# Kernel tuning notes

Measured on AMD Instinct MI355X. Metric: run time of the kernel, lower is better.

The kernel has to match this reference:

```python
import jax, jax.numpy as jnp
import numpy as np

B, N, C_IN, C_OUT, NUM_TYPES = 4, 4096, 128, 64, 5
TEMP = 1.0  # self.temp is undefined in the source; use 1.0


def setup_inputs() -> dict:
    key = jax.random.key(0)
    ks = jax.random.split(key, 9)
    bound_p = np.sqrt(6.0 / (C_IN + C_OUT))
    bound_k = np.sqrt(6.0 / (C_OUT + 1))
    return {
        "node_rep": jax.random.normal(ks[0], (B, N, C_IN), dtype=jnp.float32),
        "adj_matrix": jax.random.uniform(ks[1], (N, N), dtype=jnp.float32),
        "node_type": jax.random.randint(ks[2], (N,), 0, NUM_TYPES),
        "proj_W": jax.random.uniform(ks[3], (C_OUT, C_IN), minval=-bound_p, maxval=bound_p, dtype=jnp.float32),
        "proj_b": jnp.zeros((C_OUT,), dtype=jnp.float32),
        "k_W": jax.random.uniform(ks[4], (NUM_TYPES, C_OUT), minval=-bound_k, maxval=bound_k, dtype=jnp.float32),
        "k_b": jnp.zeros((NUM_TYPES,), dtype=jnp.float32),
        "v_W": jax.random.uniform(ks[5], (NUM_TYPES, C_OUT), minval=-bound_k, maxval=bound_k, dtype=jnp.float32),
        "v_b": jnp.zeros((NUM_TYPES,), dtype=jnp.float32),
    }


def reference(node_rep, adj_matrix, node_type, proj_W, proj_b, k_W, k_b, v_W, v_b):
    # projection: [B,N,c_in] -> [B,N,c_out]
    h = jnp.einsum('bnc,oc->bno', node_rep, proj_W) + proj_b
    # per-type scalar scores stacked: [B,N,num_types]
    ks = jnp.einsum('bno,to->bnt', h, k_W) + k_b
    vs = jnp.einsum('bno,to->bnt', h, v_W) + v_b
    # gather score of each node's own type -> [B,N,1]
    idx = jnp.broadcast_to(node_type[None, :, None], (h.shape[0], h.shape[1], 1))
    f1 = jnp.take_along_axis(ks, idx, axis=2)           # [B,N,1]
    f2 = jnp.take_along_axis(vs, idx, axis=2)           # [B,N,1]
    # pairwise logits masked/weighted by adjacency: [B,N,N]
    attn_logits = adj_matrix[None, :, :] * (f1 + jnp.swapaxes(f2, 1, 2))
    unnorm = jax.nn.sigmoid(attn_logits) - 0.5
    attn_probs = jax.nn.softmax(unnorm / TEMP, axis=1)  # softmax over dim 1, as in source
    # aggregate: [B,N,N] @ [B,N,c_out] -> [B,N,c_out]
    return jnp.matmul(attn_probs, h)
```

## Files before the change

kernel.cpp:

```cpp
#include <hip/hip_runtime.h>
#include <hip/hip_bf16.h>
#include <stdint.h>

#define NN   4096
#define BB   4
#define CIN  128
#define COUT 64
#define JSPL 4

typedef __attribute__((ext_vector_type(4))) float f32x4;
typedef __attribute__((ext_vector_type(8))) short s16x8;
typedef __attribute__((ext_vector_type(4))) int   i32x4;

__device__ __forceinline__ float sig_exp(float u) {
    const float L = 1.4426950408889634f;
    float e0 = __builtin_amdgcn_exp2f(-u * L);
    float sg = __builtin_amdgcn_rcpf(1.0f + e0);
    return __builtin_amdgcn_exp2f(__builtin_fmaf(sg, L, -0.7213475204444817f));
}

__device__ __forceinline__ short f2bf(float x) {
    unsigned u = __builtin_bit_cast(unsigned, x);
    return (short)((u + 0x8000u) >> 16);
}

__global__ __launch_bounds__(256) void k_proj(
    const float* __restrict__ node_rep, const int* __restrict__ node_type,
    const float* __restrict__ pW, const float* __restrict__ pb,
    const float* __restrict__ kW, const float* __restrict__ kb,
    const float* __restrict__ vW, const float* __restrict__ vb,
    float* __restrict__ h, float* __restrict__ f1, float* __restrict__ f2,
    float* __restrict__ denom)
{
    if (blockIdx.x < (BB * NN) / 256)
        denom[blockIdx.x * 256 + threadIdx.x] = 0.0f;

    int row = blockIdx.x * 4 + (threadIdx.x >> 6);
    int o   = threadIdx.x & 63;
    int n   = row & (NN - 1);

    const f32x4* xr = (const f32x4*)(node_rep + (size_t)row * CIN);
    const f32x4* wr = (const f32x4*)(pW + (size_t)o * CIN);
    float a0 = pb[o], a1 = 0.f, a2 = 0.f, a3 = 0.f;
    #pragma unroll
    for (int c = 0; c < CIN / 4; ++c) {
        f32x4 x = xr[c], w = wr[c];
        a0 = fmaf(x[0], w[0], a0);
        a1 = fmaf(x[1], w[1], a1);
        a2 = fmaf(x[2], w[2], a2);
        a3 = fmaf(x[3], w[3], a3);
    }
    float acc = (a0 + a1) + (a2 + a3);
    h[(size_t)row * COUT + o] = acc;

    int t = node_type[n];
    float s1 = acc * kW[t * COUT + o];
    float s2 = acc * vW[t * COUT + o];
    #pragma unroll
    for (int off = 32; off; off >>= 1) {
        s1 += __shfl_xor(s1, off, 64);
        s2 += __shfl_xor(s2, off, 64);
    }
    if (o == 0) { f1[row] = s1 + kb[t]; f2[row] = s2 + vb[t]; }
}

__global__ __launch_bounds__(256) void k_denom(
    const float* __restrict__ adj, const float* __restrict__ f1,
    const float* __restrict__ f2, float* __restrict__ denom)
{
    int j4 = blockIdx.x * 1024 + threadIdx.x * 4;
    int i0 = blockIdx.y * 16;

    f32x4 f2r[BB], acc[BB];
    #pragma unroll
    for (int b = 0; b < BB; ++b) {
        f2r[b] = *(const f32x4*)(f2 + b * NN + j4);
        acc[b] = (f32x4){0.f, 0.f, 0.f, 0.f};
    }

    const float* abase = adj + (size_t)i0 * NN + j4;
    f32x4 aA = *(const f32x4*)(abase);
    for (int ii = 0; ii < 16; ii += 2) {
        f32x4 aB = *(const f32x4*)(abase + (size_t)(ii + 1) * NN);
        #pragma unroll
        for (int b = 0; b < BB; ++b) {
            float fv = f1[b * NN + i0 + ii];
            #pragma unroll
            for (int q = 0; q < 4; ++q) acc[b][q] += sig_exp(aA[q] * (fv + f2r[b][q]));
        }
        if (ii + 2 < 16) aA = *(const f32x4*)(abase + (size_t)(ii + 2) * NN);
        #pragma unroll
        for (int b = 0; b < BB; ++b) {
            float fv = f1[b * NN + i0 + ii + 1];
            #pragma unroll
            for (int q = 0; q < 4; ++q) acc[b][q] += sig_exp(aB[q] * (fv + f2r[b][q]));
        }
    }
    #pragma unroll
    for (int b = 0; b < BB; ++b)
        #pragma unroll
        for (int q = 0; q < 4; ++q)
            atomicAdd(&denom[b * NN + j4 + q], acc[b][q]);
}

__global__ __launch_bounds__(256) void k_hst(
    const float* __restrict__ h, const float* __restrict__ denom,
    unsigned short* __restrict__ hsT)
{
    int b  = blockIdx.y;
    int j0 = blockIdx.x * 64;
    __shared__ float tile[64][65];
    int cx = threadIdx.x & 63;
    int ry = threadIdx.x >> 6;
    #pragma unroll
    for (int k = 0; k < 16; ++k) {
        int jl = k * 4 + ry;
        float rd = __builtin_amdgcn_rcpf(denom[b * NN + j0 + jl]);
        tile[jl][cx] = h[((size_t)b * NN + j0 + jl) * COUT + cx] * rd;
    }
    __syncthreads();
    #pragma unroll
    for (int k = 0; k < 16; ++k) {
        int cl = k * 4 + ry;
        hsT[((size_t)b * COUT + cl) * NN + j0 + cx] = (unsigned short)f2bf(tile[cx][cl]);
    }
}

__global__ __launch_bounds__(256, 4) void k_out(
    const float* __restrict__ adj, const float* __restrict__ f1,
    const float* __restrict__ f2, const unsigned short* __restrict__ hsT,
    float* __restrict__ pout)
{
    int i0   = blockIdx.x * 16;
    int jsp  = blockIdx.y;
    int b    = threadIdx.x >> 6;
    int lane = threadIdx.x & 63;
    int lrow = lane & 15;
    int lgrp = lane >> 4;

    const float*          arow = adj + (size_t)(i0 + lrow) * NN;
    const float*          f2b  = f2 + b * NN;
    const unsigned short* hsb  = hsT + ((size_t)b * COUT + lrow) * NN;
    float f1v = f1[b * NN + i0 + lrow];

    f32x4 acc0 = {0.f, 0.f, 0.f, 0.f};
    f32x4 acc1 = acc0, acc2 = acc0, acc3 = acc0;

    int jb = jsp * (NN / JSPL) + lgrp * 8;

#define LDAH(t, a0, a1, h0, h1, h2, h3) {                                  \
    int jk = jb + (t) * 32;                                                \
    a0 = *(const f32x4*)(arow + jk);                                       \
    a1 = *(const f32x4*)(arow + jk + 4);                                   \
    h0 = *(const i32x4*)(hsb + jk);                                        \
    h1 = *(const i32x4*)(hsb + (size_t)16 * NN + jk);                      \
    h2 = *(const i32x4*)(hsb + (size_t)32 * NN + jk);                      \
    h3 = *(const i32x4*)(hsb + (size_t)48 * NN + jk); }

#define COMP(t, a0, a1, h0, h1, h2, h3) {                                  \
    int jk = jb + (t) * 32;                                                \
    f32x4 s0 = *(const f32x4*)(f2b + jk);                                  \
    f32x4 s1 = *(const f32x4*)(f2b + jk + 4);                              \
    float e0 = sig_exp(a0[0] * (f1v + s0[0]));                             \
    float e1 = sig_exp(a0[1] * (f1v + s0[1]));                             \
    float e2 = sig_exp(a0[2] * (f1v + s0[2]));                             \
    float e3 = sig_exp(a0[3] * (f1v + s0[3]));                             \
    float e4 = sig_exp(a1[0] * (f1v + s1[0]));                             \
    float e5 = sig_exp(a1[1] * (f1v + s1[1]));                             \
    float e6 = sig_exp(a1[2] * (f1v + s1[2]));                             \
    float e7 = sig_exp(a1[3] * (f1v + s1[3]));                             \
    s16x8 af;                                                              \
    af[0] = f2bf(e0); af[1] = f2bf(e1); af[2] = f2bf(e2); af[3] = f2bf(e3);\
    af[4] = f2bf(e4); af[5] = f2bf(e5); af[6] = f2bf(e6); af[7] = f2bf(e7);\
    acc0 = __builtin_amdgcn_mfma_f32_16x16x32_bf16(af, __builtin_bit_cast(s16x8, h0), acc0, 0, 0, 0); \
    acc1 = __builtin_amdgcn_mfma_f32_16x16x32_bf16(af, __builtin_bit_cast(s16x8, h1), acc1, 0, 0, 0); \
    acc2 = __builtin_amdgcn_mfma_f32_16x16x32_bf16(af, __builtin_bit_cast(s16x8, h2), acc2, 0, 0, 0); \
    acc3 = __builtin_amdgcn_mfma_f32_16x16x32_bf16(af, __builtin_bit_cast(s16x8, h3), acc3, 0, 0, 0); }

    f32x4 Aa0, Aa1, Ba0, Ba1;
    i32x4 Ah0, Ah1, Ah2, Ah3, Bh0, Bh1, Bh2, Bh3;
    const int T = NN / JSPL / 32;
    LDAH(0, Aa0, Aa1, Ah0, Ah1, Ah2, Ah3);
    for (int t = 0; t < T; t += 2) {
        LDAH(t + 1, Ba0, Ba1, Bh0, Bh1, Bh2, Bh3);
        COMP(t, Aa0, Aa1, Ah0, Ah1, Ah2, Ah3);
        if (t + 2 < T) LDAH(t + 2, Aa0, Aa1, Ah0, Ah1, Ah2, Ah3);
        COMP(t + 1, Ba0, Ba1, Bh0, Bh1, Bh2, Bh3);
    }
#undef LDAH
#undef COMP

    #pragma unroll
    for (int r = 0; r < 4; ++r) {
        float* orow = pout + ((size_t)(jsp * BB + b) * NN + i0 + lgrp * 4 + r) * COUT + lrow;
        orow[ 0] = acc0[r];
        orow[16] = acc1[r];
        orow[32] = acc2[r];
        orow[48] = acc3[r];
    }
}

__global__ __launch_bounds__(256) void k_ored(
    const float* __restrict__ pout, float* __restrict__ out)
{
    size_t e = ((size_t)blockIdx.x * 256 + threadIdx.x) * 4;
    f32x4 s = *(const f32x4*)(pout + e);
    #pragma unroll
    for (int sp = 1; sp < JSPL; ++sp)
        s += *(const f32x4*)(pout + (size_t)sp * BB * NN * COUT + e);
    *(f32x4*)(out + e) = s;
}

extern "C" void kernel_launch(void* const* d_in, const int* in_sizes, int n_in,
                              void* d_out, int out_size, void* d_ws, size_t ws_size,
                              hipStream_t stream)
{
    const float* node_rep = (const float*)d_in[0];
    const float* adj      = (const float*)d_in[1];
    const int*   ntype    = (const int*)  d_in[2];
    const float* pW       = (const float*)d_in[3];
    const float* pb       = (const float*)d_in[4];
    const float* kW       = (const float*)d_in[5];
    const float* kb       = (const float*)d_in[6];
    const float* vW       = (const float*)d_in[7];
    const float* vb       = (const float*)d_in[8];
    float* out = (float*)d_out;

    char* w = (char*)d_ws;
    float*          h     = (float*)(w);
    float*          f1    = (float*)(w + 4194304);
    float*          f2    = (float*)(w + 4259840);
    float*          denom = (float*)(w + 4325376);
    unsigned short* hsT   = (unsigned short*)(w + 4390912);
    float*          pout  = (float*)(w + 6488064);

    k_proj <<<BB * NN / 4, 256, 0, stream>>>(node_rep, ntype, pW, pb, kW, kb, vW, vb, h, f1, f2, denom);
    k_denom<<<dim3(NN / 1024, NN / 16), 256, 0, stream>>>(adj, f1, f2, denom);
    k_hst  <<<dim3(NN / 64, BB), 256, 0, stream>>>(h, denom, hsT);
    k_out  <<<dim3(NN / 16, JSPL), 256, 0, stream>>>(adj, f1, f2, hsT, pout);
    k_ored <<<BB * NN * COUT / 1024, 256, 0, stream>>>(pout, out);
}
```

Measured before the change: 344.8 us.

## Materialize bf16 attention weights once and consume them with an MFMA GEMM

Adds a path that computes the exp(sigmoid) weights once, writes them to workspace as a bf16 matrix, and accumulates per-block partial column sums. A separate reduction kernel replaces the atomic denominator accumulation. A dedicated bf16 MFMA GEMM then multiplies the stored weights by the normalized, transposed h. This removes the second pass of transcendental work in the output kernel, at the cost of writing and reading about 128MB of extra traffic. The new path runs only if the workspace is large enough; otherwise the old kernels run.

Result: faster. 300.1 us (-13.0%).

```diff
diff --git a/kernel.cpp b/kernel.cpp
--- a/kernel.cpp
+++ b/kernel.cpp
@@ -8,9 +8,10 @@
 #define COUT 64
 #define JSPL 4
 
-typedef __attribute__((ext_vector_type(4))) float f32x4;
-typedef __attribute__((ext_vector_type(8))) short s16x8;
-typedef __attribute__((ext_vector_type(4))) int   i32x4;
+typedef __attribute__((ext_vector_type(4))) float          f32x4;
+typedef __attribute__((ext_vector_type(8))) short          s16x8;
+typedef __attribute__((ext_vector_type(4))) int            i32x4;
+typedef __attribute__((ext_vector_type(4))) unsigned short u16x4;
 
 __device__ __forceinline__ float sig_exp(float u) {
     const float L = 1.4426950408889634f;
@@ -63,6 +64,156 @@
     }
     if (o == 0) { f1[row] = s1 + kb[t]; f2[row] = s2 + vb[t]; }
 }
+
+
+__global__ __launch_bounds__(256) void k_emit(
+    const float* __restrict__ adj, const float* __restrict__ f1,
+    const float* __restrict__ f2, unsigned short* __restrict__ E,
+    float* __restrict__ pd)
+{
+    int j4 = blockIdx.x * 1024 + threadIdx.x * 4;
+    int i0 = blockIdx.y * 16;
+
+    f32x4 f2r[BB], acc[BB];
+    #pragma unroll
+    for (int b = 0; b < BB; ++b) {
+        f2r[b] = *(const f32x4*)(f2 + b * NN + j4);
+        acc[b] = (f32x4){0.f, 0.f, 0.f, 0.f};
+    }
+
+    const float* abase = adj + (size_t)i0 * NN + j4;
+    f32x4 cur = *(const f32x4*)(abase);
+    f32x4 nxt = *(const f32x4*)(abase + NN);
+
+    for (int ii = 0; ii < 16; ++ii) {
+        f32x4 a = cur;
+        cur = nxt;
+        if (ii + 2 < 16) nxt = *(const f32x4*)(abase + (size_t)(ii + 2) * NN);
+        int i = i0 + ii;
+        #pragma unroll
+        for (int b = 0; b < BB; ++b) {
+            float fv = f1[b * NN + i];
+            u16x4 ev;
+            #pragma unroll
+            for (int q = 0; q < 4; ++q) {
+                float e = sig_exp(a[q] * (fv + f2r[b][q]));
+                acc[b][q] += e;
+                ev[q] = (unsigned short)f2bf(e);
+            }
+            *(u16x4*)(E + ((size_t)b * NN + i) * NN + j4) = ev;
+        }
+    }
+    #pragma unroll
+    for (int b = 0; b < BB; ++b)
+        *(f32x4*)(pd + (size_t)(blockIdx.y * BB + b) * NN + j4) = acc[b];
+}
+
+__global__ __launch_bounds__(256) void k_dred(
+    const float* __restrict__ pd, float* __restrict__ rden)
+{
+    int gid = blockIdx.x * 256 + threadIdx.x;
+    float s0 = 0.f, s1 = 0.f, s2 = 0.f, s3 = 0.f;
+    for (int it = 0; it < 256; it += 4) {
+        s0 += pd[(size_t)(it + 0) * BB * NN + gid];
+        s1 += pd[(size_t)(it + 1) * BB * NN + gid];
+        s2 += pd[(size_t)(it + 2) * BB * NN + gid];
+        s3 += pd[(size_t)(it + 3) * BB * NN + gid];
+    }
+    rden[gid] = 1.0f / ((s0 + s1) + (s2 + s3));
+}
+
+__global__ __launch_bounds__(256) void k_hst_mul(
+    const float* __restrict__ h, const float* __restrict__ rden,
+    unsigned short* __restrict__ hsT)
+{
+    int b  = blockIdx.y;
+    int j0 = blockIdx.x * 64;
+    __shared__ float tile[64][65];
+    int cx = threadIdx.x & 63;
+    int ry = threadIdx.x >> 6;
+    #pragma unroll
+    for (int k = 0; k < 16; ++k) {
+        int jl = k * 4 + ry;
+        tile[jl][cx] = h[((size_t)b * NN + j0 + jl) * COUT + cx] * rden[b * NN + j0 + jl];
+    }
+    __syncthreads();
+    #pragma unroll
+    for (int k = 0; k < 16; ++k) {
+        int cl = k * 4 + ry;
+        hsT[((size_t)b * COUT + cl) * NN + j0 + cx] = (unsigned short)f2bf(tile[cx][cl]);
+    }
+}
+
+__global__ __launch_bounds__(512) void k_gemm(
+    const unsigned short* __restrict__ E, const unsigned short* __restrict__ hsT,
+    float* __restrict__ out)
+{
+    int i0   = blockIdx.x * 16;
+    int b    = blockIdx.y;
+    int tid  = threadIdx.x;
+    int wid  = tid >> 6;
+    int lane = tid & 63;
+    int lrow = lane & 15;
+    int lgrp = lane >> 4;
+
+    const unsigned short* ea  = E   + ((size_t)b * NN + i0 + lrow) * NN;
+    const unsigned short* hsb = hsT + ((size_t)b * COUT + lrow) * NN;
+
+    f32x4 acc0 = {0.f, 0.f, 0.f, 0.f};
+    f32x4 acc1 = acc0, acc2 = acc0, acc3 = acc0;
+
+    int kb = wid * (NN / 8) + lgrp * 8;
+
+#define LD(t, av, h0, h1, h2, h3) {                                 \
+    int jk = kb + (t) * 32;                                         \
+    av = *(const i32x4*)(ea + jk);                                  \
+    h0 = *(const i32x4*)(hsb + jk);                                 \
+    h1 = *(const i32x4*)(hsb + (size_t)16 * NN + jk);               \
+    h2 = *(const i32x4*)(hsb + (size_t)32 * NN + jk);               \
+    h3 = *(const i32x4*)(hsb + (size_t)48 * NN + jk); }
+
+#define MM(av, h0, h1, h2, h3) {                                    \
+    s16x8 af = __builtin_bit_cast(s16x8, av);                       \
+    acc0 = __builtin_amdgcn_mfma_f32_16x16x32_bf16(af, __builtin_bit_cast(s16x8, h0), acc0, 0, 0, 0); \
+    acc1 = __builtin_amdgcn_mfma_f32_16x16x32_bf16(af, __builtin_bit_cast(s16x8, h1), acc1, 0, 0, 0); \
+    acc2 = __builtin_amdgcn_mfma_f32_16x16x32_bf16(af, __builtin_bit_cast(s16x8, h2), acc2, 0, 0, 0); \
+    acc3 = __builtin_amdgcn_mfma_f32_16x16x32_bf16(af, __builtin_bit_cast(s16x8, h3), acc3, 0, 0, 0); }
+
+    i32x4 Aa, Ah0, Ah1, Ah2, Ah3, Ba, Bh0, Bh1, Bh2, Bh3;
+    const int T = NN / 8 / 32;
+    LD(0, Aa, Ah0, Ah1, Ah2, Ah3);
+    for (int t = 0; t < T; t += 2) {
+        LD(t + 1, Ba, Bh0, Bh1, Bh2, Bh3);
+        MM(Aa, Ah0, Ah1, Ah2, Ah3);
+        if (t + 2 < T) LD(t + 2, Aa, Ah0, Ah1, Ah2, Ah3);
+        MM(Ba, Bh0, Bh1, Bh2, Bh3);
+    }
+#undef LD
+#undef MM
+
+    __shared__ float red[8][16][64];
+    #pragma unroll
+    for (int r = 0; r < 4; ++r) {
+        red[wid][lgrp * 4 + r][ 0 + lrow] = acc0[r];
+        red[wid][lgrp * 4 + r][16 + lrow] = acc1[r];
+        red[wid][lgrp * 4 + r][32 + lrow] = acc2[r];
+        red[wid][lgrp * 4 + r][48 + lrow] = acc3[r];
+    }
+    __syncthreads();
+
+    int e2 = tid * 2;
+    int ii = e2 >> 6;
+    int cc = e2 & 63;
+    float sx = 0.f, sy = 0.f;
+    #pragma unroll
+    for (int w = 0; w < 8; ++w) {
+        sx += red[w][ii][cc];
+        sy += red[w][ii][cc + 1];
+    }
+    float* op = out + ((size_t)b * NN + i0 + ii) * COUT + cc;
+    op[0] = sx; op[1] = sy;
+}
+
 
 __global__ __launch_bounds__(256) void k_denom(
     const float* __restrict__ adj, const float* __restrict__ f1,
@@ -103,7 +254,7 @@
             atomicAdd(&denom[b * NN + j4 + q], acc[b][q]);
 }
 
-__global__ __launch_bounds__(256) void k_hst(
+__global__ __launch_bounds__(256) void k_hst_rcp(
     const float* __restrict__ h, const float* __restrict__ denom,
     unsigned short* __restrict__ hsT)
 {
@@ -230,13 +381,23 @@
     float*          h     = (float*)(w);
     float*          f1    = (float*)(w + 4194304);
     float*          f2    = (float*)(w + 4259840);
-    float*          denom = (float*)(w + 4325376);
+    float*          rden  = (float*)(w + 4325376);
     unsigned short* hsT   = (unsigned short*)(w + 4390912);
-    float*          pout  = (float*)(w + 6488064);
-
-    k_proj <<<BB * NN / 4, 256, 0, stream>>>(node_rep, ntype, pW, pb, kW, kb, vW, vb, h, f1, f2, denom);
-    k_denom<<<dim3(NN / 1024, NN / 16), 256, 0, stream>>>(adj, f1, f2, denom);
-    k_hst  <<<dim3(NN / 64, BB), 256, 0, stream>>>(h, denom, hsT);
-    k_out  <<<dim3(NN / 16, JSPL), 256, 0, stream>>>(adj, f1, f2, hsT, pout);
-    k_ored <<<BB * NN * COUT / 1024, 256, 0, stream>>>(pout, out);
-}
+    float*          pd    = (float*)(w + 6488064);
+    unsigned short* E     = (unsigned short*)(w + 23265280);
+    const size_t NEED = 23265280ULL + (size_t)BB * NN * NN * 2ULL;
+
+    k_proj<<<BB * NN / 4, 256, 0, stream>>>(node_rep, ntype, pW, pb, kW, kb, vW, vb, h, f1, f2, rden);
+
+    if (ws_size >= NEED) {
+        k_emit   <<<dim3(NN / 1024, NN / 16), 256, 0, stream>>>(adj, f1, f2, E, pd);
+        k_dred   <<<BB * NN / 256, 256, 0, stream>>>(pd, rden);
+        k_hst_mul<<<dim3(NN / 64, BB), 256, 0, stream>>>(h, rden, hsT);
+        k_gemm   <<<dim3(NN / 16, BB), 512, 0, stream>>>(E, hsT, out);
+    } else {
+        k_denom  <<<dim3(NN / 1024, NN / 16), 256, 0, stream>>>(adj, f1, f2, rden);
+        k_hst_rcp<<<dim3(NN / 64, BB), 256, 0, stream>>>(h, rden, hsT);
+        k_out    <<<dim3(NN / 16, JSPL), 256, 0, stream>>>(adj, f1, f2, hsT, pd);
+        k_ored   <<<BB * NN * COUT / 1024, 256, 0, stream>>>(pd, out);
+    }
+}
```
